# Kernel optimization log

Hardware: AMD Instinct MI355X
Metric: run time of the kernel (lower is better)

## Reference

```python
import jax, jax.numpy as jnp
import numpy as np

D_MODEL = 1024
NUM_HEADS = 16
D_K = D_MODEL // NUM_HEADS


def setup_inputs() -> dict:
    key = jax.random.key(0)
    ks = jax.random.split(key, 11)
    B, S = 2, 2048
    scale = 1.0 / np.sqrt(D_MODEL)
    inp = {
        "Q": jax.random.normal(ks[0], (B, S, D_MODEL), jnp.float32),
        "K": jax.random.normal(ks[1], (B, S, D_MODEL), jnp.float32),
        "V": jax.random.normal(ks[2], (B, S, D_MODEL), jnp.float32),
        "W_q": jax.random.normal(ks[3], (D_MODEL, D_MODEL), jnp.float32) * scale,
        "b_q": jnp.zeros((D_MODEL,), jnp.float32),
        "W_k": jax.random.normal(ks[4], (D_MODEL, D_MODEL), jnp.float32) * scale,
        "b_k": jnp.zeros((D_MODEL,), jnp.float32),
        "W_v": jax.random.normal(ks[5], (D_MODEL, D_MODEL), jnp.float32) * scale,
        "b_v": jnp.zeros((D_MODEL,), jnp.float32),
        "W_o": jax.random.normal(ks[6], (D_MODEL, D_MODEL), jnp.float32) * scale,
        "b_o": jnp.zeros((D_MODEL,), jnp.float32),
    }
    return inp


def _split_heads(x):
    B, S, _ = x.shape
    return x.reshape(B, S, NUM_HEADS, D_K).transpose(0, 2, 1, 3)  # [B,H,S,dk]


def reference(Q, K, V, W_q, b_q, W_k, b_k, W_v, b_v, W_o, b_o):
    # Linear projections (torch Linear: x @ W^T + b)
    q = _split_heads(Q @ W_q.T + b_q)
    k = _split_heads(K @ W_k.T + b_k)
    v = _split_heads(V @ W_v.T + b_v)
    scale = 1.0 / jnp.sqrt(jnp.float32(D_K))
    scores = jnp.einsum("bhqd,bhkd->bhqk", q, k) * scale  # [B,H,S,S]
    attn = jax.nn.softmax(scores, axis=-1)
    # dropout is identity in eval mode
    out = jnp.einsum("bhqk,bhkd->bhqd", attn, v)  # [B,H,S,dk]
    B, H, S, dk = out.shape
    out = out.transpose(0, 2, 1, 3).reshape(B, S, H * dk)
    output = out @ W_o.T + b_o
    return output, attn
```

## Files before the change

### kernel.cpp

```cpp
#include <hip/hip_runtime.h>

typedef __bf16 bf16x8 __attribute__((ext_vector_type(8)));
typedef float f32x4 __attribute__((ext_vector_type(4)));
typedef unsigned short u16x4 __attribute__((ext_vector_type(4)));
typedef unsigned short u16x8 __attribute__((ext_vector_type(8)));

#define DEV __device__ __forceinline__

DEV unsigned short f2bf(float x) {
    union { float f; unsigned u; } v; v.f = x;
    unsigned r = (v.u + 0x7FFFu + ((v.u >> 16) & 1u)) >> 16;
    return (unsigned short)r;
}
DEV float bf2f(unsigned short h) {
    union { unsigned u; float f; } v; v.u = ((unsigned)h) << 16;
    return v.f;
}
DEV void gload16(const void* g, void* l) {
    __builtin_amdgcn_global_load_lds((const __attribute__((address_space(1))) void*)g,
                                     (__attribute__((address_space(3))) void*)l, 16, 0, 0);
}

__global__ __launch_bounds__(512) void gemm_proj(
    const float* __restrict__ A0, const float* __restrict__ A1, const float* __restrict__ A2,
    const float* __restrict__ W0, const float* __restrict__ W1, const float* __restrict__ W2,
    const float* __restrict__ B0, const float* __restrict__ B1, const float* __restrict__ B2,
    unsigned short* O0, unsigned short* O1, unsigned short* O2)
{
    const int raw = blockIdx.x;
    const int f = (raw & 7) * 48 + (raw >> 3);
    const int bx = f % 8;
    const int by = (f / 8) % 16;
    const int z  = f / 128;

    const float* A       = (z == 0) ? A0 : (z == 1) ? A1 : A2;
    const float* W       = (z == 0) ? W0 : (z == 1) ? W1 : W2;
    const float* bias    = (z == 0) ? B0 : (z == 1) ? B1 : B2;
    unsigned short* outp = (z == 0) ? O0 : (z == 1) ? O1 : O2;

    __shared__ unsigned short sA[256 * 32];
    __shared__ unsigned short sB[128 * 32];

    const int tid = threadIdx.x, lane = tid & 63;
    const int wv = tid >> 6, wrow = wv >> 2, wcol = wv & 3;
    const int l15 = lane & 15, lg = lane >> 4;
    const int row0 = by * 256, col0 = bx * 128;

    f32x4 acc[8][2];
#pragma unroll
    for (int m = 0; m < 8; ++m)
#pragma unroll
        for (int n = 0; n < 2; ++n) acc[m][n] = f32x4{0.f, 0.f, 0.f, 0.f};

    const int rA = tid >> 1, cA = (tid & 1) * 16;
    const int rB = tid >> 2, cB = (tid & 3) * 8;
    const float* Abase = A + (size_t)(row0 + rA) * 1024 + cA;
    const float* Wbase = W + (size_t)(col0 + rB) * 1024 + cB;

    for (int kt = 0; kt < 32; ++kt) {
        const int kf = kt * 32;
        f32x4 a0 = *(const f32x4*)(Abase + kf);
        f32x4 a1 = *(const f32x4*)(Abase + kf + 4);
        f32x4 a2 = *(const f32x4*)(Abase + kf + 8);
        f32x4 a3 = *(const f32x4*)(Abase + kf + 12);
        f32x4 w0 = *(const f32x4*)(Wbase + kf);
        f32x4 w1 = *(const f32x4*)(Wbase + kf + 4);
        u16x8 pa0, pa1, pw;
#pragma unroll
        for (int j = 0; j < 4; ++j) {
            pa0[j] = f2bf(a0[j]); pa0[4 + j] = f2bf(a1[j]);
            pa1[j] = f2bf(a2[j]); pa1[4 + j] = f2bf(a3[j]);
            pw[j]  = f2bf(w0[j]); pw[4 + j]  = f2bf(w1[j]);
        }
        __syncthreads();
        *(u16x8*)&sA[rA * 32 + cA]     = pa0;
        *(u16x8*)&sA[rA * 32 + cA + 8] = pa1;
        *(u16x8*)&sB[rB * 32 + cB]     = pw;
        __syncthreads();

        bf16x8 af[8], bfr[2];
#pragma unroll
        for (int m = 0; m < 8; ++m) {
            int arow = wrow * 128 + m * 16 + l15;
            af[m] = *(const bf16x8*)&sA[arow * 32 + lg * 8];
        }
#pragma unroll
        for (int n = 0; n < 2; ++n) {
            int bcol = wcol * 32 + n * 16 + l15;
            bfr[n] = *(const bf16x8*)&sB[bcol * 32 + lg * 8];
        }
#pragma unroll
        for (int m = 0; m < 8; ++m)
#pragma unroll
            for (int n = 0; n < 2; ++n)
                acc[m][n] = __builtin_amdgcn_mfma_f32_16x16x32_bf16(af[m], bfr[n], acc[m][n], 0, 0, 0);
    }

#pragma unroll
    for (int m = 0; m < 8; ++m) {
#pragma unroll
        for (int n = 0; n < 2; ++n) {
            const int C = col0 + wcol * 32 + n * 16 + l15;
            const int Rbase = row0 + wrow * 128 + m * 16 + lg * 4;
            const float bv = bias[C];
            const int bq = Rbase >> 11, s0 = Rbase & 2047, hh = C >> 6, dd = C & 63;
            if (z != 2) {
                const size_t base = ((size_t)(bq * 16 + hh) * 2048 + s0) * 64 + dd;
#pragma unroll
                for (int j = 0; j < 4; ++j)
                    outp[base + (size_t)j * 64] = f2bf(acc[m][n][j] + bv);
            } else {
                const size_t base = ((size_t)(bq * 16 + hh) * 64 + dd) * 2048 + s0;
                u16x4 pk;
#pragma unroll
                for (int j = 0; j < 4; ++j) pk[j] = f2bf(acc[m][n][j] + bv);
                *(u16x4*)&outp[base] = pk;
            }
        }
    }
}

__global__ __launch_bounds__(256) void gemm_final(
    const unsigned short* __restrict__ A, const float* __restrict__ W,
    const float* __restrict__ bias, float* __restrict__ out)
{
    const int raw = blockIdx.x;
    const int f = (raw & 7) * 64 + (raw >> 3);
    const int bx = f % 16;
    const int by = f / 16;

    __shared__ unsigned short sA[128 * 32];
    __shared__ unsigned short sB[64 * 32];

    const int tid = threadIdx.x, lane = tid & 63;
    const int wv = tid >> 6, wrow = wv >> 1, wcol = wv & 1;
    const int l15 = lane & 15, lg = lane >> 4;
    const int row0 = by * 128, col0 = bx * 64;

    f32x4 acc[4][2];
#pragma unroll
    for (int m = 0; m < 4; ++m)
#pragma unroll
        for (int n = 0; n < 2; ++n) acc[m][n] = f32x4{0.f, 0.f, 0.f, 0.f};

    const char* Ab = (const char*)(A + (size_t)row0 * 1024);
    const int o1 = tid * 16, o2 = (256 + tid) * 16;
    const int r1 = o1 >> 6, c1 = o1 & 63, r2 = o2 >> 6, c2 = o2 & 63;
    const int rB = tid >> 2, cB = (tid & 3) * 8;
    const float* Wbase = W + (size_t)(col0 + rB) * 1024 + cB;

    for (int kt = 0; kt < 32; ++kt) {
        const int kb = kt * 64;
        f32x4 w0 = *(const f32x4*)(Wbase + kt * 32);
        f32x4 w1 = *(const f32x4*)(Wbase + kt * 32 + 4);
        u16x8 pw;
#pragma unroll
        for (int j = 0; j < 4; ++j) { pw[j] = f2bf(w0[j]); pw[4 + j] = f2bf(w1[j]); }
        __syncthreads();
        gload16(Ab + (size_t)r1 * 2048 + kb + c1, (char*)sA + o1);
        gload16(Ab + (size_t)r2 * 2048 + kb + c2, (char*)sA + o2);
        *(u16x8*)&sB[rB * 32 + cB] = pw;
        __syncthreads();

        bf16x8 af[4], bfr[2];
#pragma unroll
        for (int m = 0; m < 4; ++m) {
            int arow = wrow * 64 + m * 16 + l15;
            af[m] = *(const bf16x8*)&sA[arow * 32 + lg * 8];
        }
#pragma unroll
        for (int n = 0; n < 2; ++n) {
            int bcol = wcol * 32 + n * 16 + l15;
            bfr[n] = *(const bf16x8*)&sB[bcol * 32 + lg * 8];
        }
#pragma unroll
        for (int m = 0; m < 4; ++m)
#pragma unroll
            for (int n = 0; n < 2; ++n)
                acc[m][n] = __builtin_amdgcn_mfma_f32_16x16x32_bf16(af[m], bfr[n], acc[m][n], 0, 0, 0);
    }

#pragma unroll
    for (int m = 0; m < 4; ++m) {
#pragma unroll
        for (int n = 0; n < 2; ++n) {
            const int C = col0 + wcol * 32 + n * 16 + l15;
            const int Rbase = row0 + wrow * 64 + m * 16 + lg * 4;
            const float bv = bias[C];
            const size_t base = (size_t)Rbase * 1024 + C;
#pragma unroll
            for (int j = 0; j < 4; ++j)
                __builtin_nontemporal_store(acc[m][n][j] + bv, &out[base + (size_t)j * 1024]);
        }
    }
}

__global__ __launch_bounds__(512, 1) void attn_k(
    const unsigned short* __restrict__ qh, const unsigned short* __restrict__ kh,
    const unsigned short* __restrict__ vT, unsigned short* __restrict__ oa,
    float* __restrict__ attn_out)
{
    __shared__ unsigned short p[32 * 2048];
    __shared__ float Olds[2][32][64];
    __shared__ float wsum[128];
    __shared__ float rinvw[8][32];

    const int tid = threadIdx.x, lane = tid & 63, w = tid >> 6;
    const int l15 = lane & 15, lg = lane >> 4;

    const int raw = blockIdx.x;
    const int f = (raw & 7) * 256 + (raw >> 3);
    const int q0 = (f & 63) * 32;
    const int h = (f >> 6) & 15, b = f >> 10;

    const size_t headoff = (size_t)(b * 16 + h) * 131072;
    const unsigned short* qhead = qh + headoff + (size_t)q0 * 64;
    const unsigned short* khead = kh + headoff;
    const unsigned short* vhead = vT + headoff;

    const int qh_ = w >> 2, kq = w & 3;
    const int colbase = kq * 512;
    const int qrow = qh_ * 16 + l15;
    const bf16x8 aq0 = *(const bf16x8*)(qhead + qrow * 64 + lg * 8);
    const bf16x8 aq1 = *(const bf16x8*)(qhead + qrow * 64 + 32 + lg * 8);

    const unsigned short* kptr = khead + (size_t)(colbase + l15) * 64 + lg * 8;
    bf16x8 kf0 = *(const bf16x8*)(kptr);
    bf16x8 kf1 = *(const bf16x8*)(kptr + 32);
    float psum = 0.f;

    for (int t = 0; t < 32; ++t) {
        bf16x8 nk0, nk1;
        if (t < 31) {
            const unsigned short* np = kptr + (size_t)(t + 1) * 1024;
            nk0 = *(const bf16x8*)(np);
            nk1 = *(const bf16x8*)(np + 32);
        }
        f32x4 c = {0.f, 0.f, 0.f, 0.f};
        c = __builtin_amdgcn_mfma_f32_16x16x32_bf16(kf0, aq0, c, 0, 0, 0);
        c = __builtin_amdgcn_mfma_f32_16x16x32_bf16(kf1, aq1, c, 0, 0, 0);
        u16x4 pk;
#pragma unroll
        for (int j = 0; j < 4; ++j) {
            float e = __expf(c[j] * 0.125f);
            psum += e;
            pk[j] = f2bf(e);
        }
        int byte = (qrow << 12) + ((colbase + t * 16 + lg * 4) << 1);
        byte ^= (qrow & 7) << 4;
        *(u16x4*)((char*)p + byte) = pk;
        kf0 = nk0; kf1 = nk1;
    }

    psum += __shfl_xor(psum, 16);
    psum += __shfl_xor(psum, 32);
    if (lane < 16) wsum[w * 16 + lane] = psum;
    __syncthreads();

    if (lane < 32) {
        const int q = lane;
        const int base = (q >> 4) * 64 + (q & 15);
        rinvw[w][q] = 1.0f / (wsum[base] + wsum[base + 16] + wsum[base + 32] + wsum[base + 48]);
    }

    float* aout = attn_out + ((size_t)(b * 16 + h) * 2048 + q0) * 2048;
    for (int i = 0; i < 32; ++i) {
        int byte = (i << 12) + (tid << 3);
        byte ^= (i & 7) << 4;
        const u16x4 pv = *(const u16x4*)((char*)p + byte);
        const float inv = rinvw[w][i];
        f32x4 ov = { bf2f(pv[0]) * inv, bf2f(pv[1]) * inv, bf2f(pv[2]) * inv, bf2f(pv[3]) * inv };
        __builtin_nontemporal_store(ov, (f32x4*)&aout[(size_t)i * 2048 + tid * 4]);
    }

    const int dq = w & 3, kh2 = w >> 2;
    const int d0 = dq * 16;
    f32x4 acc0 = {0.f, 0.f, 0.f, 0.f}, acc1 = {0.f, 0.f, 0.f, 0.f};
    const unsigned short* vptr = vhead + (size_t)(d0 + l15) * 2048 + kh2 * 1024 + lg * 8;
    bf16x8 vf = *(const bf16x8*)(vptr);
    for (int kc = 0; kc < 32; ++kc) {
        bf16x8 nvf;
        if (kc < 31) nvf = *(const bf16x8*)(vptr + (size_t)(kc + 1) * 32);
        const int colb = (kh2 * 1024 + kc * 32 + lg * 8) << 1;
        int b0 = (l15 << 12) + colb;         b0 ^= (l15 & 7) << 4;
        int b1 = ((16 + l15) << 12) + colb;  b1 ^= (l15 & 7) << 4;
        const bf16x8 pa0 = *(const bf16x8*)((char*)p + b0);
        const bf16x8 pa1 = *(const bf16x8*)((char*)p + b1);
        acc0 = __builtin_amdgcn_mfma_f32_16x16x32_bf16(pa0, vf, acc0, 0, 0, 0);
        acc1 = __builtin_amdgcn_mfma_f32_16x16x32_bf16(pa1, vf, acc1, 0, 0, 0);
        vf = nvf;
    }
#pragma unroll
    for (int j = 0; j < 4; ++j) {
        Olds[kh2][lg * 4 + j][d0 + l15]      = acc0[j];
        Olds[kh2][16 + lg * 4 + j][d0 + l15] = acc1[j];
    }
    __syncthreads();

    {
        const int q = tid >> 4, d4 = (tid & 15) * 4;
        f32x4 s = *(const f32x4*)&Olds[0][q][d4];
        s += *(const f32x4*)&Olds[1][q][d4];
        const float rq = rinvw[w][q];
        u16x4 pk;
#pragma unroll
        for (int j = 0; j < 4; ++j) pk[j] = f2bf(s[j] * rq);
        *(u16x4*)&oa[((size_t)b * 2048 + q0 + q) * 1024 + h * 64 + d4] = pk;
    }
}

extern "C" void kernel_launch(void* const* d_in, const int* in_sizes, int n_in,
                              void* d_out, int out_size, void* d_ws, size_t ws_size,
                              hipStream_t stream) {
    const float* Q  = (const float*)d_in[0];
    const float* K  = (const float*)d_in[1];
    const float* V  = (const float*)d_in[2];
    const float* Wq = (const float*)d_in[3];
    const float* bq = (const float*)d_in[4];
    const float* Wk = (const float*)d_in[5];
    const float* bk = (const float*)d_in[6];
    const float* Wv = (const float*)d_in[7];
    const float* bv = (const float*)d_in[8];
    const float* Wo = (const float*)d_in[9];
    const float* bo = (const float*)d_in[10];

    char* ws = (char*)d_ws;
    unsigned short* qhd = (unsigned short*)(ws + 33554432);
    unsigned short* khd = (unsigned short*)(ws + 41943040);
    unsigned short* vTd = (unsigned short*)(ws + 50331648);
    unsigned short* oad = (unsigned short*)(ws + 58720256);

    float* out = (float*)d_out;
    float* attn_out = out + 4194304;

    gemm_proj<<<dim3(384), 512, 0, stream>>>(Q, K, V, Wq, Wk, Wv,
                                             bq, bk, bv, qhd, khd, vTd);

    attn_k<<<dim3(2048), 512, 0, stream>>>(qhd, khd, vTd, oad, attn_out);

    gemm_final<<<dim3(512), 256, 0, stream>>>(oad, Wo, bo, out);
}
```

Measured before the change: 297.3 us.

## Halve attention query tile to 16 rows to raise occupancy

Each attention block now handles 16 query rows instead of 32, which halves its LDS use (P buffer about 64KB instead of 128KB). The launch bound is raised to allow several blocks per CU, and the grid doubles to 4096 blocks. Every wave now covers a 256-key column slice for all 16 rows, and the row-sum reduction runs over 8 waves. The goal is to hide latency, mostly on the large attention-probability store, through higher occupancy. The cost is that K and V are reloaded twice as often per query, and the PV stage gets half the MFMA work per block, with half the threads idle in the final write.

New measurement: 330.7 us. 11.2% more time.

```diff
diff --git a/kernel.cpp b/kernel.cpp
--- a/kernel.cpp
+++ b/kernel.cpp
@@ -195,43 +195,42 @@
     }
 }
 
-__global__ __launch_bounds__(512, 1) void attn_k(
+__global__ __launch_bounds__(512, 4) void attn_k(
     const unsigned short* __restrict__ qh, const unsigned short* __restrict__ kh,
     const unsigned short* __restrict__ vT, unsigned short* __restrict__ oa,
     float* __restrict__ attn_out)
 {
-    __shared__ unsigned short p[32 * 2048];
-    __shared__ float Olds[2][32][64];
-    __shared__ float wsum[128];
-    __shared__ float rinvw[8][32];
+    __shared__ unsigned short p[16 * 2048];
+    __shared__ float Olds[2][16][64];
+    __shared__ float wsum[8][16];
+    __shared__ float rinvw[8][16];
 
     const int tid = threadIdx.x, lane = tid & 63, w = tid >> 6;
     const int l15 = lane & 15, lg = lane >> 4;
 
     const int raw = blockIdx.x;
-    const int f = (raw & 7) * 256 + (raw >> 3);
-    const int q0 = (f & 63) * 32;
-    const int h = (f >> 6) & 15, b = f >> 10;
+    const int f = (raw & 7) * 512 + (raw >> 3);
+    const int q0 = (f & 127) * 16;
+    const int h = (f >> 7) & 15, b = f >> 11;
 
     const size_t headoff = (size_t)(b * 16 + h) * 131072;
     const unsigned short* qhead = qh + headoff + (size_t)q0 * 64;
     const unsigned short* khead = kh + headoff;
     const unsigned short* vhead = vT + headoff;
 
-    const int qh_ = w >> 2, kq = w & 3;
-    const int colbase = kq * 512;
-    const int qrow = qh_ * 16 + l15;
-    const bf16x8 aq0 = *(const bf16x8*)(qhead + qrow * 64 + lg * 8);
-    const bf16x8 aq1 = *(const bf16x8*)(qhead + qrow * 64 + 32 + lg * 8);
+    const int colbase = w * 256;
+    const bf16x8 aq0 = *(const bf16x8*)(qhead + l15 * 64 + lg * 8);
+    const bf16x8 aq1 = *(const bf16x8*)(qhead + l15 * 64 + 32 + lg * 8);
 
     const unsigned short* kptr = khead + (size_t)(colbase + l15) * 64 + lg * 8;
     bf16x8 kf0 = *(const bf16x8*)(kptr);
     bf16x8 kf1 = *(const bf16x8*)(kptr + 32);
     float psum = 0.f;
 
-    for (int t = 0; t < 32; ++t) {
+#pragma unroll
+    for (int t = 0; t < 16; ++t) {
         bf16x8 nk0, nk1;
-        if (t < 31) {
+        if (t < 15) {
             const unsigned short* np = kptr + (size_t)(t + 1) * 1024;
             nk0 = *(const bf16x8*)(np);
             nk1 = *(const bf16x8*)(np + 32);
@@ -246,25 +245,25 @@
             psum += e;
             pk[j] = f2bf(e);
         }
-        int byte = (qrow << 12) + ((colbase + t * 16 + lg * 4) << 1);
-        byte ^= (qrow & 7) << 4;
+        int byte = (l15 << 12) + ((colbase + t * 16 + lg * 4) << 1);
+        byte ^= (l15 & 7) << 4;
         *(u16x4*)((char*)p + byte) = pk;
         kf0 = nk0; kf1 = nk1;
     }
 
     psum += __shfl_xor(psum, 16);
     psum += __shfl_xor(psum, 32);
-    if (lane < 16) wsum[w * 16 + lane] = psum;
+    if (lane < 16) wsum[w][lane] = psum;
     __syncthreads();
 
-    if (lane < 32) {
-        const int q = lane;
-        const int base = (q >> 4) * 64 + (q & 15);
-        rinvw[w][q] = 1.0f / (wsum[base] + wsum[base + 16] + wsum[base + 32] + wsum[base + 48]);
+    if (lane < 16) {
+        float s = wsum[0][lane] + wsum[1][lane] + wsum[2][lane] + wsum[3][lane]
+                + wsum[4][lane] + wsum[5][lane] + wsum[6][lane] + wsum[7][lane];
+        rinvw[w][lane] = 1.0f / s;
     }
 
     float* aout = attn_out + ((size_t)(b * 16 + h) * 2048 + q0) * 2048;
-    for (int i = 0; i < 32; ++i) {
+    for (int i = 0; i < 16; ++i) {
         int byte = (i << 12) + (tid << 3);
         byte ^= (i & 7) << 4;
         const u16x4 pv = *(const u16x4*)((char*)p + byte);
@@ -275,29 +274,24 @@
 
     const int dq = w & 3, kh2 = w >> 2;
     const int d0 = dq * 16;
-    f32x4 acc0 = {0.f, 0.f, 0.f, 0.f}, acc1 = {0.f, 0.f, 0.f, 0.f};
+    f32x4 acc0 = {0.f, 0.f, 0.f, 0.f};
     const unsigned short* vptr = vhead + (size_t)(d0 + l15) * 2048 + kh2 * 1024 + lg * 8;
     bf16x8 vf = *(const bf16x8*)(vptr);
     for (int kc = 0; kc < 32; ++kc) {
         bf16x8 nvf;
         if (kc < 31) nvf = *(const bf16x8*)(vptr + (size_t)(kc + 1) * 32);
-        const int colb = (kh2 * 1024 + kc * 32 + lg * 8) << 1;
-        int b0 = (l15 << 12) + colb;         b0 ^= (l15 & 7) << 4;
-        int b1 = ((16 + l15) << 12) + colb;  b1 ^= (l15 & 7) << 4;
+        int b0 = (l15 << 12) + ((kh2 * 1024 + kc * 32 + lg * 8) << 1);
+        b0 ^= (l15 & 7) << 4;
         const bf16x8 pa0 = *(const bf16x8*)((char*)p + b0);
-        const bf16x8 pa1 = *(const bf16x8*)((char*)p + b1);
         acc0 = __builtin_amdgcn_mfma_f32_16x16x32_bf16(pa0, vf, acc0, 0, 0, 0);
-        acc1 = __builtin_amdgcn_mfma_f32_16x16x32_bf16(pa1, vf, acc1, 0, 0, 0);
         vf = nvf;
     }
 #pragma unroll
-    for (int j = 0; j < 4; ++j) {
-        Olds[kh2][lg * 4 + j][d0 + l15]      = acc0[j];
-        Olds[kh2][16 + lg * 4 + j][d0 + l15] = acc1[j];
-    }
+    for (int j = 0; j < 4; ++j)
+        Olds[kh2][lg * 4 + j][d0 + l15] = acc0[j];
     __syncthreads();
 
-    {
+    if (tid < 256) {
         const int q = tid >> 4, d4 = (tid & 15) * 4;
         f32x4 s = *(const f32x4*)&Olds[0][q][d4];
         s += *(const f32x4*)&Olds[1][q][d4];
@@ -336,7 +330,7 @@
     gemm_proj<<<dim3(384), 512, 0, stream>>>(Q, K, V, Wq, Wk, Wv,
                                              bq, bk, bv, qhd, khd, vTd);
 
-    attn_k<<<dim3(2048), 512, 0, stream>>>(qhd, khd, vTd, oad, attn_out);
+    attn_k<<<dim3(4096), 512, 0, stream>>>(qhd, khd, vTd, oad, attn_out);
 
     gemm_final<<<dim3(512), 256, 0, stream>>>(oad, Wo, bo, out);
 }
```
